# Performance work log

Hardware: AMD Instinct MI355X
Metric: run time of the kernel (lower is better)

## Reference

```python
import jax, jax.numpy as jnp
import numpy as np

D_MODEL = 160
D_STATE = 64
D_CONV = 12
N_BLOCKS = 8
D_INNER = 2 * D_MODEL          # expand=2
DT_RANK = (D_MODEL + 15) // 16 # math.ceil(d_model/16) = 10
K_PRE = 9
B, L = 8, 512


def setup_inputs() -> dict:
    key = jax.random.key(0)
    ks = jax.random.split(key, 12)
    f = lambda k, shape, s=0.02: jax.random.normal(k, shape, jnp.float32) * s
    return {
        "x": jax.random.normal(ks[0], (B, L, 1), jnp.float32),
        "pre_w": f(ks[1], (D_MODEL, 1, K_PRE), 0.3),
        "pre_b": f(ks[2], (D_MODEL,), 0.1),
        "ln_w": jnp.ones((N_BLOCKS, D_MODEL), jnp.float32),
        "ln_b": jnp.zeros((N_BLOCKS, D_MODEL), jnp.float32),
        "in_proj_w": f(ks[3], (N_BLOCKS, 2 * D_INNER, D_MODEL)),
        "conv_w": f(ks[4], (N_BLOCKS, D_INNER, 1, D_CONV), 0.2),
        "conv_b": f(ks[5], (N_BLOCKS, D_INNER), 0.1),
        "x_proj_w": f(ks[6], (N_BLOCKS, DT_RANK + 2 * D_STATE, D_INNER)),
        "dt_proj_w": f(ks[7], (N_BLOCKS, D_INNER, DT_RANK), 0.1),
        "dt_proj_b": jax.random.uniform(ks[8], (N_BLOCKS, D_INNER), jnp.float32, -4.0, -2.0),
        "A_log": jnp.log(jnp.broadcast_to(jnp.arange(1, D_STATE + 1, dtype=jnp.float32), (N_BLOCKS, D_INNER, D_STATE))),
        "D_skip": jnp.ones((N_BLOCKS, D_INNER), jnp.float32),
        "out_proj_w": f(ks[9], (N_BLOCKS, D_MODEL, D_INNER)),
        "head_w": f(ks[10], (1, D_MODEL), 0.05),
        "head_b": jnp.zeros((1,), jnp.float32),
    }


def _layernorm(x, w, b, eps=1e-5):
    mu = x.mean(-1, keepdims=True)
    var = x.var(-1, keepdims=True)  # torch LayerNorm uses biased variance
    return (x - mu) / jnp.sqrt(var + eps) * w + b


def _causal_dwconv(x, w, b):
    # x: (B, L, C); w: (C, 1, K) depthwise; causal: pad left K-1, keep first L
    y = jax.lax.conv_general_dilated(
        x.transpose(0, 2, 1), w, (1,), [(w.shape[-1] - 1, 0)],
        feature_group_count=w.shape[0], dimension_numbers=("NCH", "OIH", "NCH"))
    return (y + b[None, :, None]).transpose(0, 2, 1)


def _selective_scan(u, dt, A, Bm, Cm, D):
    # u, dt: (B, L, d); A: (d, n); Bm, Cm: (B, L, n); D: (d,)
    def step(h, inp):
        u_t, dt_t, B_t, C_t = inp              # (B,d) (B,d) (B,n) (B,n)
        dA = jnp.exp(dt_t[:, :, None] * A)      # (B, d, n)
        h = dA * h + (dt_t * u_t)[:, :, None] * B_t[:, None, :]
        y = jnp.einsum("bdn,bn->bd", h, C_t)
        return h, y

    h0 = jnp.zeros((u.shape[0], A.shape[0], A.shape[1]), u.dtype)
    xs = (u.transpose(1, 0, 2), dt.transpose(1, 0, 2),
          Bm.transpose(1, 0, 2), Cm.transpose(1, 0, 2))
    _, ys = jax.lax.scan(step, h0, xs)          # ys: (L, B, d)
    return ys.transpose(1, 0, 2) + u * D


def _mamba(x, p):
    xz = jnp.einsum("bld,ed->ble", x, p["in_proj_w"])  # (B, L, 2*d_inner)
    u, z = jnp.split(xz, 2, axis=-1)
    u = jax.nn.silu(_causal_dwconv(u, p["conv_w"], p["conv_b"]))
    dbl = jnp.einsum("bld,ed->ble", u, p["x_proj_w"])  # (B, L, dt_rank+2n)
    dtr = dbl[..., :DT_RANK]
    Bm = dbl[..., DT_RANK:DT_RANK + D_STATE]
    Cm = dbl[..., DT_RANK + D_STATE:]
    dt = jax.nn.softplus(jnp.einsum("blr,dr->bld", dtr, p["dt_proj_w"]) + p["dt_proj_b"])
    A = -jnp.exp(p["A_log"])
    y = _selective_scan(u, dt, A, Bm, Cm, p["D_skip"])
    y = y * jax.nn.silu(z)
    return jnp.einsum("bld,ed->ble", y, p["out_proj_w"])


def _forward(x, pre_w, pre_b, ln_w, ln_b, in_proj_w, conv_w, conv_b,
             x_proj_w, dt_proj_w, dt_proj_b, A_log, D_skip, out_proj_w,
             head_w, head_b):
    # pre_conv: 'same' padding conv1d(1 -> d_model), then exact GELU
    h = jax.lax.conv_general_dilated(
        x.transpose(0, 2, 1), pre_w, (1,), [(K_PRE // 2, K_PRE // 2)],
        dimension_numbers=("NCH", "OIH", "NCH"))
    h = jax.nn.gelu((h + pre_b[None, :, None]).transpose(0, 2, 1), approximate=False)
    names = dict(in_proj_w=in_proj_w, conv_w=conv_w, conv_b=conv_b,
                 x_proj_w=x_proj_w, dt_proj_w=dt_proj_w, dt_proj_b=dt_proj_b,
                 A_log=A_log, D_skip=D_skip, out_proj_w=out_proj_w)
    for i in range(N_BLOCKS):  # residual Mamba blocks (dropout is identity at eval)
        p = {k: v[i] for k, v in names.items()}
        h = h + _mamba(_layernorm(h, ln_w[i], ln_b[i]), p)
    out = jnp.einsum("bld,od->blo", h, head_w) + head_b
    return out[..., 0]  # squeeze(-1) -> (B, L)


def reference(x, pre_w, pre_b, ln_w, ln_b, in_proj_w, conv_w, conv_b,
              x_proj_w, dt_proj_w, dt_proj_b, A_log, D_skip, out_proj_w,
              head_w, head_b):
    return _forward(x, pre_w, pre_b, ln_w, ln_b, in_proj_w, conv_w, conv_b,
                    x_proj_w, dt_proj_w, dt_proj_b, A_log, D_skip, out_proj_w,
                    head_w, head_b)
```

## Files before the change

### kernel.cpp

```cpp
#include <hip/hip_runtime.h>
#include <hip/hip_bf16.h>
#include <math.h>

constexpr int BB   = 8;
constexpr int LS   = 512;
constexpr int DM   = 160;
constexpr int DS   = 64;
constexpr int DC   = 12;
constexpr int NB   = 8;
constexpr int DI   = 320;
constexpr int DTR  = 10;
constexpr int KP   = 9;
constexpr int ML   = BB * LS;
constexpr int CH   = 16;
constexpr int NC   = LS / CH;
constexpr int NPAD = 192;

#define LOG2E 1.44269504088896340736f

#if defined(__has_builtin)
#if __has_builtin(__builtin_amdgcn_exp2f)
#define EXP2(x) __builtin_amdgcn_exp2f(x)
#endif
#endif
#ifndef EXP2
#define EXP2(x) exp2f(x)
#endif

typedef __attribute__((ext_vector_type(8))) short bf16x8;
typedef __attribute__((ext_vector_type(4))) float f32x4;

__device__ __forceinline__ unsigned short f2bf(float f) {
    unsigned int u = __builtin_bit_cast(unsigned int, f);
    u = (u + 0x7fffu + ((u >> 16) & 1u)) >> 16;
    return (unsigned short)u;
}
__device__ __forceinline__ float bf2f(unsigned short s) {
    unsigned int u = ((unsigned int)s) << 16;
    return __builtin_bit_cast(float, u);
}

constexpr int T_IN = NB * 2 * DI * DM;
constexpr int T_XP = NB * NPAD * DI;
constexpr int T_OP = NB * NPAD * DI;
constexpr int T_CW = NB * DC * DI;
constexpr int T_ALL = T_IN + T_XP + T_OP + T_CW;
constexpr int CVT_BLOCKS = (T_ALL + 255) / 256;

__global__ void __launch_bounds__(256)
k_prep(const float* __restrict__ x, const float* __restrict__ pw,
       const float* __restrict__ pb, const float* __restrict__ lw,
       const float* __restrict__ lb, float* __restrict__ h,
       unsigned short* __restrict__ xn,
       const float* __restrict__ w_in, const float* __restrict__ w_xp,
       const float* __restrict__ w_op, const float* __restrict__ w_cv,
       unsigned short* __restrict__ o_in, unsigned short* __restrict__ o_xp,
       unsigned short* __restrict__ o_op, float* __restrict__ o_cw) {
    __shared__ float red4[4];
    int tid = threadIdx.x;
    if (blockIdx.x < ML) {
        int row = blockIdx.x;
        int l = row & (LS - 1), b = row >> 9;
        float g = 0.f;
        if (tid < DM) {
            float acc = pb[tid];
            const float* xb = x + b * LS;
#pragma unroll
            for (int k = 0; k < KP; k++) {
                int ll = l + k - KP / 2;
                float xv = (ll >= 0 && ll < LS) ? xb[ll] : 0.f;
                acc = fmaf(xv, pw[tid * KP + k], acc);
            }
            g = 0.5f * acc * (1.f + erff(acc * 0.70710678118654752f));
            h[(size_t)row * DM + tid] = g;
        }
        float p = g;
#pragma unroll
        for (int o = 32; o; o >>= 1) p += __shfl_xor(p, o);
        if ((tid & 63) == 0) red4[tid >> 6] = p;
        __syncthreads();
        float mu = (red4[0] + red4[1] + red4[2] + red4[3]) * (1.f / DM);
        float dv = (tid < DM) ? (g - mu) : 0.f;
        float q = dv * dv;
#pragma unroll
        for (int o = 32; o; o >>= 1) q += __shfl_xor(q, o);
        __syncthreads();
        if ((tid & 63) == 0) red4[tid >> 6] = q;
        __syncthreads();
        float var = (red4[0] + red4[1] + red4[2] + red4[3]) * (1.f / DM);
        float rstd = rsqrtf(var + 1e-5f);
        if (tid < DM)
            xn[(size_t)row * DM + tid] = f2bf(dv * rstd * lw[tid] + lb[tid]);
    } else {
        int idx = (blockIdx.x - ML) * 256 + tid;
        if (idx < T_IN) { o_in[idx] = f2bf(w_in[idx]); return; }
        idx -= T_IN;
        if (idx < T_XP) {
            int k = idx % DI;
            int n = (idx / DI) % NPAD;
            int nb = idx / (DI * NPAD);
            float v = (n < 138) ? w_xp[((size_t)nb * 138 + n) * DI + k] : 0.f;
            o_xp[idx] = f2bf(v);
            return;
        }
        idx -= T_XP;
        if (idx < T_OP) {
            int k = idx % DI;
            int n = (idx / DI) % NPAD;
            int nb = idx / (DI * NPAD);
            float v = (n < DM) ? w_op[((size_t)nb * DM + n) * DI + k] : 0.f;
            o_op[idx] = f2bf(v);
            return;
        }
        idx -= T_OP;
        if (idx < T_CW) {
            int d = idx % DI;
            int k = (idx / DI) % DC;
            int nb = idx / (DI * DC);
            o_cw[idx] = w_cv[((size_t)nb * DI + d) * DC + k];
        }
    }
}

__global__ void __launch_bounds__(256)
k_ixc(const unsigned short* __restrict__ xn, const unsigned short* __restrict__ win,
      const float* __restrict__ cwT, const float* __restrict__ cb,
      const unsigned short* __restrict__ wxb,
      float* __restrict__ zbuf, unsigned short* __restrict__ u_bf,
      float* __restrict__ dtr, unsigned short* __restrict__ bc_bf) {
    __shared__ float xzu[27][DI];
    __shared__ unsigned short uA[16][DI + 8];
    int tid = threadIdx.x;
    int wave = tid >> 6, lane = tid & 63;
    int m0 = blockIdx.x * 16;
    int bseq = m0 & ~(LS - 1);
    int mstart = m0 - 11;
    int lr = lane & 15, lk = (lane >> 4) * 8;
    int drow = (lane >> 4) * 4;

    {
        f32x4 acc[2][10];
#pragma unroll
        for (int i = 0; i < 2; i++)
#pragma unroll
            for (int j = 0; j < 10; j++) acc[i][j] = (f32x4){0.f, 0.f, 0.f, 0.f};
#pragma unroll
        for (int k0 = 0; k0 < DM; k0 += 32) {
            bf16x8 a[2], b[10];
#pragma unroll
            for (int i = 0; i < 2; i++) {
                int g = mstart + i * 16 + lr;
                g = g < 0 ? 0 : (g >= ML ? ML - 1 : g);
                a[i] = *(const bf16x8*)(xn + (size_t)g * DM + k0 + lk);
            }
#pragma unroll
            for (int j = 0; j < 10; j++)
                b[j] = *(const bf16x8*)(win + (size_t)(wave * 160 + j * 16 + lr) * DM + k0 + lk);
#pragma unroll
            for (int i = 0; i < 2; i++)
#pragma unroll
                for (int j = 0; j < 10; j++)
                    acc[i][j] = __builtin_amdgcn_mfma_f32_16x16x32_bf16(a[i], b[j], acc[i][j], 0, 0, 0);
        }
#pragma unroll
        for (int i = 0; i < 2; i++) {
#pragma unroll
            for (int j = 0; j < 10; j++) {
                int col = wave * 160 + j * 16 + lr;
#pragma unroll
                for (int r = 0; r < 4; r++) {
                    int rl = i * 16 + drow + r;
                    if (rl >= 27) continue;
                    int g = mstart + rl;
                    if (col < DI) {
                        xzu[rl][col] = (g >= bseq) ? acc[i][j][r] : 0.f;
                    } else if (rl >= 11) {
                        zbuf[(size_t)g * DI + (col - DI)] = acc[i][j][r];
                    }
                }
            }
        }
    }
    __syncthreads();
    for (int idx = tid; idx < 16 * DI; idx += 256) {
        int r = idx / DI;
        int d = idx % DI;
        float acc = cb[d];
#pragma unroll
        for (int k = 0; k < DC; k++)
            acc = fmaf(xzu[r + k][d], cwT[k * DI + d], acc);
        float s = acc / (1.f + expf(-acc));
        unsigned short ub = f2bf(s);
        uA[r][d] = ub;
        u_bf[(size_t)(m0 + r) * DI + d] = ub;
    }
    __syncthreads();
    {
        f32x4 acc2[3];
#pragma unroll
        for (int j = 0; j < 3; j++) acc2[j] = (f32x4){0.f, 0.f, 0.f, 0.f};
        const unsigned short* Wb = wxb + (size_t)(wave * 48 + lr) * DI + lk;
#pragma unroll
        for (int k0 = 0; k0 < DI; k0 += 32) {
            bf16x8 a = *(const bf16x8*)&uA[lr][k0 + lk];
            bf16x8 b[3];
#pragma unroll
            for (int j = 0; j < 3; j++)
                b[j] = *(const bf16x8*)(Wb + (size_t)j * 16 * DI + k0);
#pragma unroll
            for (int j = 0; j < 3; j++)
                acc2[j] = __builtin_amdgcn_mfma_f32_16x16x32_bf16(a, b[j], acc2[j], 0, 0, 0);
        }
#pragma unroll
        for (int j = 0; j < 3; j++) {
            int gn = wave * 48 + j * 16 + lr;
            if (gn >= 138) continue;
#pragma unroll
            for (int r = 0; r < 4; r++) {
                int row = m0 + drow + r;
                float v = acc2[j][r];
                if (gn < DTR) dtr[(size_t)row * DTR + gn] = v;
                else          bc_bf[(size_t)row * 128 + (gn - DTR)] = f2bf(v);
            }
        }
    }
}

template <int MODE>
__global__ void __launch_bounds__(256)
k_oproj(const unsigned short* __restrict__ Abf, const unsigned short* __restrict__ wob,
        float* __restrict__ h, const float* __restrict__ w2, const float* __restrict__ b2,
        void* __restrict__ out2) {
    __shared__ float hl[16][164];
    int tid = threadIdx.x;
    int m0 = blockIdx.x * 16;
    int wave = tid >> 6, lane = tid & 63;
    int lr = lane & 15, lk = (lane >> 4) * 8;
    f32x4 acc[3];
#pragma unroll
    for (int j = 0; j < 3; j++) acc[j] = (f32x4){0.f, 0.f, 0.f, 0.f};
    const unsigned short* Ab = Abf + (size_t)(m0 + lr) * DI + lk;
    const unsigned short* Wb = wob + (size_t)(wave * 48 + lr) * DI + lk;
#pragma unroll
    for (int k0 = 0; k0 < DI; k0 += 32) {
        bf16x8 a = *(const bf16x8*)(Ab + k0);
        bf16x8 b[3];
#pragma unroll
        for (int j = 0; j < 3; j++)
            b[j] = *(const bf16x8*)(Wb + (size_t)j * 16 * DI + k0);
#pragma unroll
        for (int j = 0; j < 3; j++)
            acc[j] = __builtin_amdgcn_mfma_f32_16x16x32_bf16(a, b[j], acc[j], 0, 0, 0);
    }
    int drow = (lane >> 4) * 4;
#pragma unroll
    for (int j = 0; j < 3; j++) {
        int gn = wave * 48 + j * 16 + lr;
        if (gn >= DM) continue;
#pragma unroll
        for (int r = 0; r < 4; r++) {
            size_t off = (size_t)(m0 + drow + r) * DM + gn;
            float nv = h[off] + acc[j][r];
            h[off] = nv;
            hl[drow + r][gn] = nv;
        }
    }
    __syncthreads();
#pragma unroll
    for (int rr = 0; rr < 4; rr++) {
        int row = wave * 4 + rr;
        float v0 = hl[row][lane];
        float v1 = hl[row][64 + lane];
        float v2 = (lane < DM - 128) ? hl[row][128 + lane] : 0.f;
        if (MODE == 0) {
            float s = v0 + v1 + v2;
#pragma unroll
            for (int o = 32; o; o >>= 1) s += __shfl_xor(s, o);
            float mu = s * (1.f / DM);
            float q = (v0 - mu) * (v0 - mu) + (v1 - mu) * (v1 - mu);
            if (lane < DM - 128) q += (v2 - mu) * (v2 - mu);
#pragma unroll
            for (int o = 32; o; o >>= 1) q += __shfl_xor(q, o);
            float rstd = rsqrtf(q * (1.f / DM) + 1e-5f);
            unsigned short* xr = (unsigned short*)out2 + (size_t)(m0 + row) * DM;
            xr[lane]      = f2bf((v0 - mu) * rstd * w2[lane]      + b2[lane]);
            xr[64 + lane] = f2bf((v1 - mu) * rstd * w2[64 + lane] + b2[64 + lane]);
            if (lane < DM - 128)
                xr[128 + lane] = f2bf((v2 - mu) * rstd * w2[128 + lane] + b2[128 + lane]);
        } else {
            float s = v0 * w2[lane] + v1 * w2[64 + lane];
            if (lane < DM - 128) s += v2 * w2[128 + lane];
#pragma unroll
            for (int o = 32; o; o >>= 1) s += __shfl_xor(s, o);
            if (lane == 0) ((float*)out2)[m0 + row] = s + b2[0];
        }
    }
}

#define MAKE_DA(dA, t2, qoff)                                   \
    float e1 = EXP2(t2);                                        \
    float p0 = EXP2(t2 * qoff);                                 \
    float e2 = e1 * e1, e4 = e2 * e2;                           \
    dA[0] = p0; dA[1] = p0 * e1; dA[2] = p0 * e2; dA[3] = dA[1] * e2; \
    _Pragma("unroll")                                           \
    for (int kq = 4; kq < 16; kq++) dA[kq] = dA[kq - 4] * e4;

__device__ __forceinline__ float dt_of(const float* __restrict__ dtr, const float* __restrict__ wdt,
                                       const float* __restrict__ bdt, int row, int dd) {
    const float* r = dtr + (size_t)row * DTR;
    const float* w = wdt + dd * DTR;
    float acc = bdt[dd];
#pragma unroll
    for (int k = 0; k < DTR; k++) acc = fmaf(r[k], w[k], acc);
    return fmaxf(acc, 0.f) + log1pf(expf(-fabsf(acc)));
}

__global__ void k_scanA(const unsigned short* __restrict__ u_bf, const float* __restrict__ dtr,
                        const unsigned short* __restrict__ bc_bf,
                        const float* __restrict__ wdt, const float* __restrict__ bdt,
                        unsigned short* __restrict__ HE, float* __restrict__ S) {
    __shared__ float sB[CH][64];
    __shared__ float sDT[CH][64];
    __shared__ float sBC[CH][64];
    int tid = threadIdx.x;
    int q = tid >> 6, dl = tid & 63;
    int dbase = blockIdx.x * 64;
    int d = dbase + dl;
    int c = blockIdx.y, b = blockIdx.z;
    int row0 = b * LS + c * CH;
    for (int i = tid; i < CH * 64; i += 256) {
        int st = i >> 6, j = i & 63;
        sB[st][j] = bf2f(bc_bf[(size_t)(row0 + st) * 128 + j]);
    }
    for (int i = tid; i < CH * 64; i += 256) {
        int st = i >> 6, j = i & 63;
        int dd = dbase + j;
        float sp = dt_of(dtr, wdt, bdt, row0 + st, dd);
        float uv = bf2f(u_bf[(size_t)(row0 + st) * DI + dd]);
        sDT[st][j] = sp;
        sBC[st][j] = sp * uv;
    }
    __syncthreads();
    if (q == 0) {
        float s = 0.f;
#pragma unroll
        for (int t = 0; t < CH; t++) s += sDT[t][dl];
        S[(size_t)(b * NC + c) * DI + d] = s;
    }
    float qoff = (float)(q * 16 + 1);
    float h[16];
#pragma unroll
    for (int k = 0; k < 16; k++) h[k] = 0.f;
    for (int t = 0; t < CH; t++) {
        float dtv = sDT[t][dl];
        float bc  = sBC[t][dl];
        float t2 = -dtv * LOG2E;
        float dA[16];
        MAKE_DA(dA, t2, qoff)
#pragma unroll
        for (int k = 0; k < 16; k++)
            h[k] = fmaf(dA[k], h[k], bc * sB[t][q * 16 + k]);
    }
    size_t base = ((size_t)(b * NC + c) * DS + q * 16) * DI + d;
#pragma unroll
    for (int k = 0; k < 16; k++) HE[base + (size_t)k * DI] = f2bf(h[k]);
}

__global__ void k_scanB(const float* __restrict__ Alog, const float* __restrict__ S,
                        unsigned short* __restrict__ HE) {
    int gid = blockIdx.x * blockDim.x + threadIdx.x;
    if (gid >= BB * DS * DI) return;
    int d = gid % DI;
    int n = (gid / DI) % DS;
    int b = gid / (DI * DS);
    float a2 = -expf(Alog[(size_t)d * DS + n]) * LOG2E;
    float h = 0.f;
    size_t idx  = ((size_t)(b * NC) * DS + n) * DI + d;
    size_t sidx = (size_t)(b * NC) * DI + d;
    float e = bf2f(HE[idx]), s = S[sidx];
    for (int c = 0; c < NC; c++) {
        float en = 0.f, sn = 0.f;
        if (c + 1 < NC) {
            en = bf2f(HE[idx + (size_t)DS * DI]);
            sn = S[sidx + DI];
        }
        HE[idx] = f2bf(h);
        h = EXP2(a2 * s) * h + e;
        e = en; s = sn;
        idx += (size_t)DS * DI; sidx += DI;
    }
}

__global__ void k_scanC(const unsigned short* __restrict__ u_bf, const float* __restrict__ dtr,
                        const unsigned short* __restrict__ bc_bf,
                        const float* __restrict__ wdt, const float* __restrict__ bdt,
                        const float* __restrict__ Dskip, const float* __restrict__ zbuf,
                        const unsigned short* __restrict__ HE, unsigned short* __restrict__ y_bf) {
    __shared__ float sB[CH][64];
    __shared__ float sC[CH][64];
    __shared__ float sDT[CH][64];
    __shared__ float sU[CH][64];
    __shared__ float ylds[4][CH][64];
    int tid = threadIdx.x;
    int q = tid >> 6, dl = tid & 63;
    int dbase = blockIdx.x * 64;
    int d = dbase + dl;
    int c = blockIdx.y, b = blockIdx.z;
    int row0 = b * LS + c * CH;
    for (int i = tid; i < CH * 128; i += 256) {
        int st = i >> 7, j = i & 127;
        float v = bf2f(bc_bf[(size_t)(row0 + st) * 128 + j]);
        if (j < 64) sB[st][j] = v;
        else        sC[st][j - 64] = v;
    }
    for (int i = tid; i < CH * 64; i += 256) {
        int st = i >> 6, j = i & 63;
        int dd = dbase + j;
        sDT[st][j] = dt_of(dtr, wdt, bdt, row0 + st, dd);
        sU[st][j]  = bf2f(u_bf[(size_t)(row0 + st) * DI + dd]);
    }
    float h[16];
    size_t base = ((size_t)(b * NC + c) * DS + q * 16) * DI + d;
#pragma unroll
    for (int k = 0; k < 16; k++) h[k] = bf2f(HE[base + (size_t)k * DI]);
    float Dv = (q == 0) ? Dskip[d] : 0.f;
    float qoff = (float)(q * 16 + 1);
    __syncthreads();
    for (int t = 0; t < CH; t++) {
        float dtv = sDT[t][dl];
        float uv  = sU[t][dl];
        float bc  = dtv * uv;
        float t2 = -dtv * LOG2E;
        float dA[16];
        MAKE_DA(dA, t2, qoff)
        float y0 = (q == 0) ? uv * Dv : 0.f, y1 = 0.f;
#pragma unroll
        for (int k = 0; k < 16; k += 2) {
            h[k]     = fmaf(dA[k],     h[k],     bc * sB[t][q * 16 + k]);
            h[k + 1] = fmaf(dA[k + 1], h[k + 1], bc * sB[t][q * 16 + k + 1]);
            y0 = fmaf(h[k],     sC[t][q * 16 + k],     y0);
            y1 = fmaf(h[k + 1], sC[t][q * 16 + k + 1], y1);
        }
        ylds[q][t][dl] = y0 + y1;
    }
    __syncthreads();
#pragma unroll
    for (int tt = 0; tt < 4; tt++) {
        int t = q * 4 + tt;
        int row = row0 + t;
        float yv = (ylds[0][t][dl] + ylds[1][t][dl]) + (ylds[2][t][dl] + ylds[3][t][dl]);
        float zv = zbuf[(size_t)row * DI + d];
        float sz = zv / (1.f + expf(-zv));
        y_bf[(size_t)row * DI + d] = f2bf(yv * sz);
    }
}

extern "C" void kernel_launch(void* const* d_in, const int* in_sizes, int n_in,
                              void* d_out, int out_size, void* d_ws, size_t ws_size,
                              hipStream_t stream) {
    const float* x         = (const float*)d_in[0];
    const float* pre_w     = (const float*)d_in[1];
    const float* pre_b     = (const float*)d_in[2];
    const float* ln_w      = (const float*)d_in[3];
    const float* ln_b      = (const float*)d_in[4];
    const float* in_proj_w = (const float*)d_in[5];
    const float* conv_w    = (const float*)d_in[6];
    const float* conv_b    = (const float*)d_in[7];
    const float* x_proj_w  = (const float*)d_in[8];
    const float* dt_proj_w = (const float*)d_in[9];
    const float* dt_proj_b = (const float*)d_in[10];
    const float* A_log     = (const float*)d_in[11];
    const float* D_skip    = (const float*)d_in[12];
    const float* out_proj_w= (const float*)d_in[13];
    const float* head_w    = (const float*)d_in[14];
    const float* head_b    = (const float*)d_in[15];
    float* out = (float*)d_out;

    float* ws = (float*)d_ws;
    float* h    = ws;
    float* zbuf = h    + (size_t)ML * DM;
    float* dtr  = zbuf + (size_t)ML * DI;
    float* S    = dtr  + (size_t)ML * DTR;
    float* cwT  = S    + (size_t)BB * NC * DI;
    unsigned short* us = (unsigned short*)(cwT + (size_t)NB * DC * DI);
    unsigned short* HE    = us;
    unsigned short* bc_bf = HE + (size_t)BB * NC * DS * DI;
    unsigned short* xn_bf = bc_bf + (size_t)ML * 128;
    unsigned short* u_bf  = xn_bf + (size_t)ML * DM;
    unsigned short* y_bf  = u_bf  + (size_t)ML * DI;
    unsigned short* win_bf = y_bf + (size_t)ML * DI;
    unsigned short* wx_bf  = win_bf + (size_t)NB * 2 * DI * DM;
    unsigned short* wo_bf  = wx_bf  + (size_t)NB * NPAD * DI;

    k_prep<<<ML + CVT_BLOCKS, 256, 0, stream>>>(x, pre_w, pre_b, ln_w, ln_b, h, xn_bf,
                                                in_proj_w, x_proj_w, out_proj_w, conv_w,
                                                win_bf, wx_bf, wo_bf, cwT);

    for (int i = 0; i < NB; i++) {
        const float* cb  = conv_b + (size_t)i * DI;
        const float* wdt = dt_proj_w + (size_t)i * DI * DTR;
        const float* bdt = dt_proj_b + (size_t)i * DI;
        const float* al  = A_log + (size_t)i * DI * DS;
        const float* dsk = D_skip + (size_t)i * DI;
        const float* cwt = cwT + (size_t)i * DC * DI;
        const unsigned short* wib = win_bf + (size_t)i * 2 * DI * DM;
        const unsigned short* wxb = wx_bf + (size_t)i * NPAD * DI;
        const unsigned short* wob = wo_bf + (size_t)i * NPAD * DI;

        k_ixc<<<ML / 16, 256, 0, stream>>>(xn_bf, wib, cwt, cb, wxb, zbuf, u_bf, dtr, bc_bf);
        {
            dim3 gA(DI / 64, NC - 1, BB);
            k_scanA<<<gA, 256, 0, stream>>>(u_bf, dtr, bc_bf, wdt, bdt, HE, S);
            k_scanB<<<(BB * DS * DI + 255) / 256, 256, 0, stream>>>(al, S, HE);
            dim3 gC(DI / 64, NC, BB);
            k_scanC<<<gC, 256, 0, stream>>>(u_bf, dtr, bc_bf, wdt, bdt, dsk, zbuf, HE, y_bf);
        }
        if (i < NB - 1) {
            k_oproj<0><<<ML / 16, 256, 0, stream>>>(y_bf, wob, h,
                                                    ln_w + (i + 1) * DM, ln_b + (i + 1) * DM,
                                                    (void*)xn_bf);
        } else {
            k_oproj<1><<<ML / 16, 256, 0, stream>>>(y_bf, wob, h, head_w, head_b, (void*)out);
        }
    }
}
```

Measured before the change: 624.8 us.

## Fuse out-projection, residual, LayerNorm into next block's in-proj/conv/x-proj kernel

Merges the previous block's out-projection, residual add and LayerNorm into the following block's in-projection, depthwise conv and x-projection kernel. Each tile recomputes an 11-row halo of out-proj and LayerNorm so the causal conv can run without a grid-wide dependency. The residual stream is ping-ponged between two buffers so blocks reading halo rows never see updated values. This saves one launch per block and the xn_bf round-trip through global memory, at the cost of redundant halo work (32 rows computed for 16 outputs) and higher shared memory and register use.

```diff
diff --git a/kernel.cpp b/kernel.cpp
--- a/kernel.cpp
+++ b/kernel.cpp
@@ -226,11 +226,185 @@
     }
 }
 
-template <int MODE>
 __global__ void __launch_bounds__(256)
-k_oproj(const unsigned short* __restrict__ Abf, const unsigned short* __restrict__ wob,
-        float* __restrict__ h, const float* __restrict__ w2, const float* __restrict__ b2,
-        void* __restrict__ out2) {
+k_oixc(const unsigned short* __restrict__ y_bf, const unsigned short* __restrict__ wob,
+       const float* __restrict__ h_in, float* __restrict__ h_out,
+       const float* __restrict__ lw, const float* __restrict__ lb,
+       const unsigned short* __restrict__ win,
+       const float* __restrict__ cwT, const float* __restrict__ cb,
+       const unsigned short* __restrict__ wxb,
+       float* __restrict__ zbuf, unsigned short* __restrict__ u_bf,
+       float* __restrict__ dtr, unsigned short* __restrict__ bc_bf) {
+    __shared__ float xzu[27][DI];
+    __shared__ unsigned short xnl[32][DM + 8];
+    __shared__ __align__(16) char smemU[32 * 164 * 4];
+    float (*hl)[164] = (float(*)[164])smemU;
+    unsigned short (*uA)[DI + 8] = (unsigned short(*)[DI + 8])smemU;
+
+    int tid = threadIdx.x;
+    int wave = tid >> 6, lane = tid & 63;
+    int m0 = blockIdx.x * 16;
+    int bseq = m0 & ~(LS - 1);
+    int mstart = m0 - 11;
+    int lr = lane & 15, lk = (lane >> 4) * 8;
+    int drow = (lane >> 4) * 4;
+
+    {
+        f32x4 acc[2][3];
+#pragma unroll
+        for (int i = 0; i < 2; i++)
+#pragma unroll
+            for (int j = 0; j < 3; j++) acc[i][j] = (f32x4){0.f, 0.f, 0.f, 0.f};
+        const unsigned short* Wb = wob + (size_t)(wave * 48 + lr) * DI + lk;
+#pragma unroll
+        for (int k0 = 0; k0 < DI; k0 += 32) {
+            bf16x8 a[2], b[3];
+#pragma unroll
+            for (int i = 0; i < 2; i++) {
+                int g = mstart + i * 16 + lr;
+                g = g < 0 ? 0 : (g >= ML ? ML - 1 : g);
+                a[i] = *(const bf16x8*)(y_bf + (size_t)g * DI + k0 + lk);
+            }
+#pragma unroll
+            for (int j = 0; j < 3; j++)
+                b[j] = *(const bf16x8*)(Wb + (size_t)j * 16 * DI + k0);
+#pragma unroll
+            for (int i = 0; i < 2; i++)
+#pragma unroll
+                for (int j = 0; j < 3; j++)
+                    acc[i][j] = __builtin_amdgcn_mfma_f32_16x16x32_bf16(a[i], b[j], acc[i][j], 0, 0, 0);
+        }
+#pragma unroll
+        for (int i = 0; i < 2; i++) {
+#pragma unroll
+            for (int j = 0; j < 3; j++) {
+                int gn = wave * 48 + j * 16 + lr;
+                if (gn >= DM) continue;
+#pragma unroll
+                for (int r = 0; r < 4; r++) {
+                    int rl = i * 16 + drow + r;
+                    int g = mstart + rl;
+                    int gc = g < 0 ? 0 : (g >= ML ? ML - 1 : g);
+                    float nv = h_in[(size_t)gc * DM + gn] + acc[i][j][r];
+                    hl[rl][gn] = nv;
+                    if (rl >= 11 && rl < 27)
+                        h_out[(size_t)g * DM + gn] = nv;
+                }
+            }
+        }
+    }
+    __syncthreads();
+#pragma unroll
+    for (int rr = 0; rr < 8; rr++) {
+        int row = wave * 8 + rr;
+        float v0 = hl[row][lane];
+        float v1 = hl[row][64 + lane];
+        float v2 = (lane < DM - 128) ? hl[row][128 + lane] : 0.f;
+        float s = v0 + v1 + v2;
+#pragma unroll
+        for (int o = 32; o; o >>= 1) s += __shfl_xor(s, o);
+        float mu = s * (1.f / DM);
+        float q = (v0 - mu) * (v0 - mu) + (v1 - mu) * (v1 - mu);
+        if (lane < DM - 128) q += (v2 - mu) * (v2 - mu);
+#pragma unroll
+        for (int o = 32; o; o >>= 1) q += __shfl_xor(q, o);
+        float rstd = rsqrtf(q * (1.f / DM) + 1e-5f);
+        xnl[row][lane]      = f2bf((v0 - mu) * rstd * lw[lane]      + lb[lane]);
+        xnl[row][64 + lane] = f2bf((v1 - mu) * rstd * lw[64 + lane] + lb[64 + lane]);
+        if (lane < DM - 128)
+            xnl[row][128 + lane] = f2bf((v2 - mu) * rstd * lw[128 + lane] + lb[128 + lane]);
+    }
+    __syncthreads();
+    {
+        f32x4 acc[2][10];
+#pragma unroll
+        for (int i = 0; i < 2; i++)
+#pragma unroll
+            for (int j = 0; j < 10; j++) acc[i][j] = (f32x4){0.f, 0.f, 0.f, 0.f};
+#pragma unroll
+        for (int k0 = 0; k0 < DM; k0 += 32) {
+            bf16x8 a[2], b[10];
+#pragma unroll
+            for (int i = 0; i < 2; i++)
+                a[i] = *(const bf16x8*)&xnl[i * 16 + lr][k0 + lk];
+#pragma unroll
+            for (int j = 0; j < 10; j++)
+                b[j] = *(const bf16x8*)(win + (size_t)(wave * 160 + j * 16 + lr) * DM + k0 + lk);
+#pragma unroll
+            for (int i = 0; i < 2; i++)
+#pragma unroll
+                for (int j = 0; j < 10; j++)
+                    acc[i][j] = __builtin_amdgcn_mfma_f32_16x16x32_bf16(a[i], b[j], acc[i][j], 0, 0, 0);
+        }
+        __syncthreads();
+#pragma unroll
+        for (int i = 0; i < 2; i++) {
+#pragma unroll
+            for (int j = 0; j < 10; j++) {
+                int col = wave * 160 + j * 16 + lr;
+#pragma unroll
+                for (int r = 0; r < 4; r++) {
+                    int rl = i * 16 + drow + r;
+                    if (rl >= 27) continue;
+                    int g = mstart + rl;
+                    if (col < DI) {
+                        xzu[rl][col] = (g >= bseq) ? acc[i][j][r] : 0.f;
+                    } else if (rl >= 11) {
+                        zbuf[(size_t)g * DI + (col - DI)] = acc[i][j][r];
+                    }
+                }
+            }
+        }
+    }
+    __syncthreads();
+    for (int idx = tid; idx < 16 * DI; idx += 256) {
+        int r = idx / DI;
+        int d = idx % DI;
+        float acc = cb[d];
+#pragma unroll
+        for (int k = 0; k < DC; k++)
+            acc = fmaf(xzu[r + k][d], cwT[k * DI + d], acc);
+        float s = acc / (1.f + expf(-acc));
+        unsigned short ub = f2bf(s);
+        uA[r][d] = ub;
+        u_bf[(size_t)(m0 + r) * DI + d] = ub;
+    }
+    __syncthreads();
+    {
+        f32x4 acc2[3];
+#pragma unroll
+        for (int j = 0; j < 3; j++) acc2[j] = (f32x4){0.f, 0.f, 0.f, 0.f};
+        const unsigned short* Wb = wxb + (size_t)(wave * 48 + lr) * DI + lk;
+#pragma unroll
+        for (int k0 = 0; k0 < DI; k0 += 32) {
+            bf16x8 a = *(const bf16x8*)&uA[lr][k0 + lk];
+            bf16x8 b[3];
+#pragma unroll
+            for (int j = 0; j < 3; j++)
+                b[j] = *(const bf16x8*)(Wb + (size_t)j * 16 * DI + k0);
+#pragma unroll
+            for (int j = 0; j < 3; j++)
+                acc2[j] = __builtin_amdgcn_mfma_f32_16x16x32_bf16(a, b[j], acc2[j], 0, 0, 0);
+        }
+#pragma unroll
+        for (int j = 0; j < 3; j++) {
+            int gn = wave * 48 + j * 16 + lr;
+            if (gn >= 138) continue;
+#pragma unroll
+            for (int r = 0; r < 4; r++) {
+                int row = m0 + drow + r;
+                float v = acc2[j][r];
+                if (gn < DTR) dtr[(size_t)row * DTR + gn] = v;
+                else          bc_bf[(size_t)row * 128 + (gn - DTR)] = f2bf(v);
+            }
+        }
+    }
+}
+
+__global__ void __launch_bounds__(256)
+k_oproj_head(const unsigned short* __restrict__ Abf, const unsigned short* __restrict__ wob,
+             float* __restrict__ h, const float* __restrict__ w2, const float* __restrict__ b2,
+             float* __restrict__ out2) {
     __shared__ float hl[16][164];
     int tid = threadIdx.x;
     int m0 = blockIdx.x * 16;
@@ -261,7 +435,6 @@
         for (int r = 0; r < 4; r++) {
             size_t off = (size_t)(m0 + drow + r) * DM + gn;
             float nv = h[off] + acc[j][r];
-            h[off] = nv;
             hl[drow + r][gn] = nv;
         }
     }
@@ -272,28 +445,11 @@
         float v0 = hl[row][lane];
         float v1 = hl[row][64 + lane];
         float v2 = (lane < DM - 128) ? hl[row][128 + lane] : 0.f;
-        if (MODE == 0) {
-            float s = v0 + v1 + v2;
-#pragma unroll
-            for (int o = 32; o; o >>= 1) s += __shfl_xor(s, o);
-            float mu = s * (1.f / DM);
-            float q = (v0 - mu) * (v0 - mu) + (v1 - mu) * (v1 - mu);
-            if (lane < DM - 128) q += (v2 - mu) * (v2 - mu);
-#pragma unroll
-            for (int o = 32; o; o >>= 1) q += __shfl_xor(q, o);
-            float rstd = rsqrtf(q * (1.f / DM) + 1e-5f);
-            unsigned short* xr = (unsigned short*)out2 + (size_t)(m0 + row) * DM;
-            xr[lane]      = f2bf((v0 - mu) * rstd * w2[lane]      + b2[lane]);
-            xr[64 + lane] = f2bf((v1 - mu) * rstd * w2[64 + lane] + b2[64 + lane]);
-            if (lane < DM - 128)
-                xr[128 + lane] = f2bf((v2 - mu) * rstd * w2[128 + lane] + b2[128 + lane]);
-        } else {
-            float s = v0 * w2[lane] + v1 * w2[64 + lane];
-            if (lane < DM - 128) s += v2 * w2[128 + lane];
-#pragma unroll
-            for (int o = 32; o; o >>= 1) s += __shfl_xor(s, o);
-            if (lane == 0) ((float*)out2)[m0 + row] = s + b2[0];
-        }
+        float s = v0 * w2[lane] + v1 * w2[64 + lane];
+        if (lane < DM - 128) s += v2 * w2[128 + lane];
+#pragma unroll
+        for (int o = 32; o; o >>= 1) s += __shfl_xor(s, o);
+        if (lane == 0) out2[m0 + row] = s + b2[0];
     }
 }
 
@@ -477,8 +633,9 @@
     float* out = (float*)d_out;
 
     float* ws = (float*)d_ws;
-    float* h    = ws;
-    float* zbuf = h    + (size_t)ML * DM;
+    float* hA   = ws;
+    float* hB   = hA   + (size_t)ML * DM;
+    float* zbuf = hB   + (size_t)ML * DM;
     float* dtr  = zbuf + (size_t)ML * DI;
     float* S    = dtr  + (size_t)ML * DTR;
     float* cwT  = S    + (size_t)BB * NC * DI;
@@ -492,10 +649,11 @@
     unsigned short* wx_bf  = win_bf + (size_t)NB * 2 * DI * DM;
     unsigned short* wo_bf  = wx_bf  + (size_t)NB * NPAD * DI;
 
-    k_prep<<<ML + CVT_BLOCKS, 256, 0, stream>>>(x, pre_w, pre_b, ln_w, ln_b, h, xn_bf,
+    k_prep<<<ML + CVT_BLOCKS, 256, 0, stream>>>(x, pre_w, pre_b, ln_w, ln_b, hA, xn_bf,
                                                 in_proj_w, x_proj_w, out_proj_w, conv_w,
                                                 win_bf, wx_bf, wo_bf, cwT);
 
+    float* hbuf[2] = {hA, hB};
     for (int i = 0; i < NB; i++) {
         const float* cb  = conv_b + (size_t)i * DI;
         const float* wdt = dt_proj_w + (size_t)i * DI * DTR;
@@ -505,9 +663,18 @@
         const float* cwt = cwT + (size_t)i * DC * DI;
         const unsigned short* wib = win_bf + (size_t)i * 2 * DI * DM;
         const unsigned short* wxb = wx_bf + (size_t)i * NPAD * DI;
-        const unsigned short* wob = wo_bf + (size_t)i * NPAD * DI;
-
-        k_ixc<<<ML / 16, 256, 0, stream>>>(xn_bf, wib, cwt, cb, wxb, zbuf, u_bf, dtr, bc_bf);
+
+        if (i == 0) {
+            k_ixc<<<ML / 16, 256, 0, stream>>>(xn_bf, wib, cwt, cb, wxb,
+                                               zbuf, u_bf, dtr, bc_bf);
+        } else {
+            const unsigned short* wob_prev = wo_bf + (size_t)(i - 1) * NPAD * DI;
+            k_oixc<<<ML / 16, 256, 0, stream>>>(y_bf, wob_prev,
+                                                hbuf[(i - 1) & 1], hbuf[i & 1],
+                                                ln_w + (size_t)i * DM, ln_b + (size_t)i * DM,
+                                                wib, cwt, cb, wxb,
+                                                zbuf, u_bf, dtr, bc_bf);
+        }
         {
             dim3 gA(DI / 64, NC - 1, BB);
             k_scanA<<<gA, 256, 0, stream>>>(u_bf, dtr, bc_bf, wdt, bdt, HE, S);
@@ -515,12 +682,7 @@
             dim3 gC(DI / 64, NC, BB);
             k_scanC<<<gC, 256, 0, stream>>>(u_bf, dtr, bc_bf, wdt, bdt, dsk, zbuf, HE, y_bf);
         }
-        if (i < NB - 1) {
-            k_oproj<0><<<ML / 16, 256, 0, stream>>>(y_bf, wob, h,
-                                                    ln_w + (i + 1) * DM, ln_b + (i + 1) * DM,
-                                                    (void*)xn_bf);
-        } else {
-            k_oproj<1><<<ML / 16, 256, 0, stream>>>(y_bf, wob, h, head_w, head_b, (void*)out);
-        }
-    }
-}
+    }
+    k_oproj_head<<<ML / 16, 256, 0, stream>>>(y_bf, wo_bf + (size_t)(NB - 1) * NPAD * DI,
+                                              hbuf[(NB - 1) & 1], head_w, head_b, out);
+}
```

After: 657.0 us. 5.2% more time.
